# Performance work log

Hardware: AMD Instinct MI355X
Metric: run time of the kernel (lower is better)

The kernel has to match this reference:

```python
import jax, jax.numpy as jnp
import numpy as np
from math import factorial, sqrt

LMAX = 2
NB = 32
NRBF = 20
CUTOFF = 5.0
N_ATOMS = 20000
N_EDGES = 400000
T = 2
M = (LMAX + 1) ** 2
LIDX = np.repeat(np.arange(LMAX + 1), 2 * np.arange(LMAX + 1) + 1)  # l of each flat (l,m) index


def _cg_complex(j1, m1, j2, m2, j3, m3):
    # Racah formula for complex-SH Clebsch-Gordan coefficients
    if m3 != m1 + m2 or j3 < abs(j1 - j2) or j3 > j1 + j2:
        return 0.0
    f = factorial
    pref = sqrt((2 * j3 + 1) * f(j1 + j2 - j3) * f(j1 - j2 + j3) * f(-j1 + j2 + j3) / f(j1 + j2 + j3 + 1))
    pref *= sqrt(f(j1 + m1) * f(j1 - m1) * f(j2 + m2) * f(j2 - m2) * f(j3 + m3) * f(j3 - m3))
    kmin = max(0, j2 - j3 - m1, j1 + m2 - j3)
    kmax = min(j1 + j2 - j3, j1 - m1, j2 + m2)
    s = 0.0
    for k in range(kmin, kmax + 1):
        s += (-1) ** k / (f(k) * f(j1 + j2 - j3 - k) * f(j1 - m1 - k) * f(j2 + m2 - k) * f(j3 - j2 + m1 + k) * f(j3 - j1 - m2 + k))
    return pref * s


def _u_matrix(l):
    # real-SH = U @ complex-SH (rows: real m from -l..l, cols: complex m')
    U = np.zeros((2 * l + 1, 2 * l + 1), dtype=np.complex128)
    for m in range(-l, l + 1):
        if m == 0:
            U[l, l] = 1.0
        elif m > 0:
            U[l + m, l + m] = (-1) ** m / sqrt(2)
            U[l + m, l - m] = 1.0 / sqrt(2)
        else:
            mu = -m
            U[l + m, l + m] = 1j / sqrt(2)
            U[l + m, l - m] = -1j * (-1) ** mu / sqrt(2)
    return U


def _build_cg_rsh(lmax):
    # CG coefficients in the real-SH basis, parity invariant (odd l1+l2+l3 blocks zero)
    cg = np.zeros((M, M, M), dtype=np.float64)
    Us = [_u_matrix(l) for l in range(lmax + 1)]
    for l1 in range(lmax + 1):
        for l2 in range(lmax + 1):
            for l3 in range(lmax + 1):
                if (l1 + l2 + l3) % 2 == 1 or l3 < abs(l1 - l2) or l3 > l1 + l2:
                    continue
                Cc = np.zeros((2 * l1 + 1, 2 * l2 + 1, 2 * l3 + 1), dtype=np.complex128)
                for i, m1 in enumerate(range(-l1, l1 + 1)):
                    for j, m2 in enumerate(range(-l2, l2 + 1)):
                        m3 = m1 + m2
                        if abs(m3) <= l3:
                            Cc[i, j, l3 + m3] = _cg_complex(l1, m1, l2, m2, l3, m3)
                R = np.einsum('ai,bj,ck,ijk->abc', Us[l1], Us[l2], np.conj(Us[l3]), Cc)
                cg[l1 * l1:(l1 + 1) ** 2, l2 * l2:(l2 + 1) ** 2, l3 * l3:(l3 + 1) ** 2] = np.real(R)
    return cg.astype(np.float32)


CG = jnp.asarray(_build_cg_rsh(LMAX))   # [9, 9, 9]
LIDX_J = jnp.asarray(LIDX)


def _rsh(dirs):
    # real spherical harmonics up to l=2 on unit vectors, flat (l,m) order -> [P, 9]
    x, y, z = dirs[:, 0], dirs[:, 1], dirs[:, 2]
    c1 = 0.4886025119029199
    c2 = 1.0925484305920792
    return jnp.stack([
        jnp.full_like(x, 0.28209479177387814),
        c1 * y, c1 * z, c1 * x,
        c2 * x * y, c2 * y * z,
        0.31539156525252005 * (3.0 * z * z - 1.0),
        c2 * x * z,
        0.5462742152960396 * (x * x - y * y),
    ], axis=1)


def _forward(atomic_numbers, r_ij, idx_i, idx_j, emb, Wf, bf, Wm1, Wm2, Wm3, Wg, bg):
    d = jnp.linalg.norm(r_ij, axis=1)                      # [P]
    Y = _rsh(r_ij / d[:, None])                            # [P, 9]
    offsets = jnp.linspace(0.0, CUTOFF, NRBF)
    width = CUTOFF / (NRBF - 1)
    radial = jnp.exp(-0.5 / width ** 2 * (d[:, None] - offsets) ** 2)   # GaussianRBF [P, NRBF]
    fcut = jnp.where(d < CUTOFF, 0.5 * (jnp.cos(d * jnp.pi / CUTOFF) + 1.0), 0.0)  # CosineCutoff
    x0 = emb[atomic_numbers]                               # nuclear embedding [N, NB]
    x = jnp.concatenate([x0[:, None, :], jnp.zeros((x0.shape[0], M - 1, NB), x0.dtype)], axis=1)  # scalar2rsh
    for t in range(T):
        # SO3Convolution: per-edge radial filter per output degree l, cutoff gated
        Wl = ((radial @ Wf[t].T + bf[t]) * fcut[:, None]).reshape(-1, LMAX + 1, NB)
        xj = x[idx_j]                                      # gather neighbors [P, 9, NB]
        tbc = jnp.einsum('pa,abc->pbc', Y, CG)             # contract Y_ij with CG
        yij = jnp.einsum('pbc,pbn->pcn', tbc, xj) * Wl[:, LIDX_J, :]
        dx = jax.ops.segment_sum(yij, idx_i, num_segments=x.shape[0], indices_are_sorted=True)
        ddx = jnp.einsum('xcn,kn->xck', dx, Wm1[t])        # mixing1 (no bias)
        dx = dx + jnp.einsum('abc,xan,xbn->xcn', CG, dx, ddx)  # SO3TensorProduct
        dx = jnp.einsum('xcn,kn->xck', dx, Wm2[t])         # mixing2
        h = jax.nn.sigmoid((dx[:, 0, :] @ Wg[t].T + bg[t]).reshape(-1, LMAX + 1, NB))
        dx = dx * h[:, LIDX_J, :]                          # SO3ParametricGatedNonlinearity
        dx = jnp.einsum('xcn,kn->xck', dx, Wm3[t])         # mixing3
        x = x + dx
    return x                                               # multipole representation [N, 9, NB]


def setup_inputs():
    key = jax.random.key(0)
    ks = jax.random.split(key, 12)
    return {
        'atomic_numbers': jax.random.randint(ks[0], (N_ATOMS,), 1, 100),
        'r_ij': jax.random.normal(ks[1], (N_EDGES, 3), jnp.float32),
        'idx_i': jnp.sort(jax.random.randint(ks[2], (N_EDGES,), 0, N_ATOMS)),
        'idx_j': jax.random.randint(ks[3], (N_EDGES,), 0, N_ATOMS),
        'emb': jax.random.normal(ks[4], (101, NB), jnp.float32).at[0].set(0.0),
        'Wf': jax.random.normal(ks[5], (T, (LMAX + 1) * NB, NRBF), jnp.float32) / sqrt(NRBF),
        'bf': jnp.zeros((T, (LMAX + 1) * NB), jnp.float32),
        'Wm1': jax.random.normal(ks[6], (T, NB, NB), jnp.float32) / sqrt(NB),
        'Wm2': jax.random.normal(ks[7], (T, NB, NB), jnp.float32) / sqrt(NB),
        'Wm3': jax.random.normal(ks[8], (T, NB, NB), jnp.float32) / sqrt(NB),
        'Wg': jax.random.normal(ks[9], (T, (LMAX + 1) * NB, NB), jnp.float32) / sqrt(NB),
        'bg': jnp.zeros((T, (LMAX + 1) * NB), jnp.float32),
    }


def reference(atomic_numbers, r_ij, idx_i, idx_j, emb, Wf, bf, Wm1, Wm2, Wm3, Wg, bg):
    return _forward(atomic_numbers, r_ij, idx_i, idx_j, emb, Wf, bf, Wm1, Wm2, Wm3, Wg, bg)
```

## Files before the change

kernel.cpp:

```cpp
#include <hip/hip_runtime.h>

#define CHUNK 16

constexpr double CFACT[8] = {1.,1.,2.,6.,24.,120.,720.,5040.};

constexpr double csqrt(double x){
  if (x <= 0.0) return 0.0;
  double s = 1.0;
  while (x > 4.0)  { x *= 0.25; s *= 2.0; }
  while (x < 0.25) { x *= 4.0;  s *= 0.5; }
  double g = 1.0;
  for (int i=0;i<10;i++) g = 0.5*(g + x/g);
  return s*g;
}

constexpr double cg_complex(int j1,int m1,int j2,int m2,int j3,int m3){
  if (m3 != m1+m2 || j3 < (j1>j2?j1-j2:j2-j1) || j3 > j1+j2) return 0.0;
  double pref = csqrt((2.0*j3+1.0)*CFACT[j1+j2-j3]*CFACT[j1-j2+j3]*CFACT[-j1+j2+j3]/CFACT[j1+j2+j3+1]);
  pref *= csqrt(CFACT[j1+m1]*CFACT[j1-m1]*CFACT[j2+m2]*CFACT[j2-m2]*CFACT[j3+m3]*CFACT[j3-m3]);
  int kmin = 0;
  if (j2-j3-m1 > kmin) kmin = j2-j3-m1;
  if (j1+m2-j3 > kmin) kmin = j1+m2-j3;
  int kmax = j1+j2-j3;
  if (j1-m1 < kmax) kmax = j1-m1;
  if (j2+m2 < kmax) kmax = j2+m2;
  double s = 0.0;
  for (int k=kmin;k<=kmax;++k){
    double t = 1.0/(CFACT[k]*CFACT[j1+j2-j3-k]*CFACT[j1-m1-k]*CFACT[j2+m2-k]*CFACT[j3-j2+m1+k]*CFACT[j3-j1-m2+k]);
    s += (k&1)? -t : t;
  }
  return pref*s;
}

struct UR { int n; int mc[2]; double re[2]; double im[2]; };
constexpr UR u_row(int m){
  UR u{}; const double is2 = 0.70710678118654752440;
  if (m==0){ u.n=1; u.mc[0]=0; u.re[0]=1.0; u.im[0]=0.0; u.mc[1]=0; u.re[1]=0.0; u.im[1]=0.0; }
  else if (m>0){ u.n=2; u.mc[0]=m;  u.re[0]=((m&1)? -is2:is2); u.im[0]=0.0;
                        u.mc[1]=-m; u.re[1]=is2;               u.im[1]=0.0; }
  else { int mu=-m; u.n=2; u.mc[0]=m;  u.re[0]=0.0; u.im[0]=is2;
                           u.mc[1]=mu; u.re[1]=0.0; u.im[1]=((mu&1)? is2:-is2); }
  return u;
}

struct CGTab { float v[9][9][9]; };
constexpr CGTab build_cg(){
  CGTab g{};
  double cc[9][9][9] = {};
  for (int a=0;a<9;a++){
    int l1 = (a==0)?0:((a<4)?1:2); int m1 = a - (l1*l1+l1);
    for (int b=0;b<9;b++){
      int l2 = (b==0)?0:((b<4)?1:2); int m2 = b - (l2*l2+l2);
      int m3 = m1+m2;
      for (int l3=0;l3<=2;l3++){
        if (m3 < -l3 || m3 > l3) continue;
        cc[a][b][l3*l3+l3+m3] = cg_complex(l1,m1,l2,m2,l3,m3);
      }
    }
  }
  for (int l1=0;l1<=2;l1++) for (int l2=0;l2<=2;l2++) for (int l3=0;l3<=2;l3++){
    if (((l1+l2+l3)&1)==1) continue;
    int dl = (l1>l2)?(l1-l2):(l2-l1);
    if (l3 < dl || l3 > l1+l2) continue;
    for (int m1=-l1;m1<=l1;m1++) for (int m2=-l2;m2<=l2;m2++) for (int m3=-l3;m3<=l3;m3++){
      UR ua = u_row(m1), ub = u_row(m2), uc = u_row(m3);
      double acc = 0.0;
      for (int i=0;i<ua.n;i++) for (int j=0;j<ub.n;j++){
        double zr = ua.re[i]*ub.re[j] - ua.im[i]*ub.im[j];
        double zi = ua.re[i]*ub.im[j] + ua.im[i]*ub.re[j];
        for (int k=0;k<uc.n;k++){
          double rp = zr*uc.re[k] + zi*uc.im[k];
          if (rp != 0.0)
            acc += rp * cc[l1*l1+l1+ua.mc[i]][l2*l2+l2+ub.mc[j]][l3*l3+l3+uc.mc[k]];
        }
      }
      g.v[l1*l1+l1+m1][l2*l2+l2+m2][l3*l3+l3+m3] = (float)acc;
    }
  }
  return g;
}
constexpr CGTab CGT = build_cg();

__global__ void init_x_kernel(const int* __restrict__ Z, const float* __restrict__ emb,
                              float4* __restrict__ x4, float4* __restrict__ dx4, int n_atoms){
  int i = blockIdx.x*blockDim.x + threadIdx.x;
  if (i >= n_atoms*72) return;
  int atom = i/72, rem = i - atom*72;
  float4 v = make_float4(0.f,0.f,0.f,0.f);
  if (rem < 8) v = reinterpret_cast<const float4*>(emb)[Z[atom]*8 + rem];
  x4[i] = v;
  dx4[i] = make_float4(0.f,0.f,0.f,0.f);
}

template<bool FIRST>
__global__ __launch_bounds__(256) void edge_kernel(
    const float* __restrict__ r_ij, const int* __restrict__ idx_i, const int* __restrict__ idx_j,
    const float* __restrict__ x, const float* __restrict__ Wf_t, const float* __restrict__ bf_t,
    float* __restrict__ dx, int n_edges)
{
  int tid = threadIdx.x;
  int g = tid >> 5, lane = tid & 31;

  int base = (blockIdx.x*8 + g)*CHUNK;
  if (base >= n_edges) return;

  int pidx;
  {
    int e0 = base + (lane & 15);
    if (e0 > n_edges-1) e0 = n_edges-1;
    pidx = (lane < 16) ? idx_i[e0] : idx_j[e0];
  }
  float rv0, rv1;
  {
    long long rmax = (long long)n_edges*3 - 1;
    long long a0 = (long long)base*3 + lane;       if (a0 > rmax) a0 = rmax;
    long long a1 = (long long)base*3 + 32 + lane;  if (a1 > rmax) a1 = rmax;
    rv0 = r_ij[a0];
    rv1 = r_ij[a1];
  }

  float wfr[3][20]; float bfl[3];
  #pragma unroll
  for (int l=0;l<3;l++){
    const float* rp = Wf_t + (l*32+lane)*20;
    #pragma unroll
    for (int q=0;q<5;q++){
      float4 v4 = *reinterpret_cast<const float4*>(rp + q*4);
      wfr[l][q*4+0]=v4.x; wfr[l][q*4+1]=v4.y; wfr[l][q*4+2]=v4.z; wfr[l][q*4+3]=v4.w;
    }
    bfl[l] = bf_t[l*32+lane];
  }

  const float STEP  = 5.0f/19.0f;
  const float ALPHA = -0.5f/(STEP*STEP);
  float myoff = (float)lane * STEP;

  float racc[9];
  #pragma unroll
  for (int c=0;c<9;c++) racc[c]=0.f;
  int cur_i = -1;

  float xjn[9];
  float xjn0;
  {
    int j0 = __shfl(pidx, 16, 32);
    const float* xp = x + j0*288 + lane;
    if (FIRST){
      xjn0 = xp[0];
    } else {
      #pragma unroll
      for (int b=0;b<9;b++) xjn[b] = xp[b*32];
    }
  }

  #pragma unroll
  for (int k=0;k<CHUNK;k++){
    int e = base + k;
    if (e >= n_edges) break;

    float xj[9]; float xj0;
    if (FIRST){
      xj0 = xjn0;
    } else {
      #pragma unroll
      for (int b=0;b<9;b++) xj[b] = xjn[b];
    }

    if (k+1 < CHUNK){
      int jn = __shfl(pidx, 16+k+1, 32);
      const float* xp = x + jn*288 + lane;
      if (FIRST){
        xjn0 = xp[0];
      } else {
        #pragma unroll
        for (int b=0;b<9;b++) xjn[b] = xp[b*32];
      }
    }

    int ii = __shfl(pidx, k, 32);

    float rx = (3*k+0 < 32) ? __shfl(rv0, 3*k+0, 32) : __shfl(rv1, 3*k+0-32, 32);
    float ry = (3*k+1 < 32) ? __shfl(rv0, 3*k+1, 32) : __shfl(rv1, 3*k+1-32, 32);
    float rz = (3*k+2 < 32) ? __shfl(rv0, 3*k+2, 32) : __shfl(rv1, 3*k+2-32, 32);

    float d2 = fmaf(rx,rx,fmaf(ry,ry,rz*rz));
    float dd = sqrtf(d2);
    float inv = __fdividef(1.0f, dd);
    float X = rx*inv, Yv = ry*inv, Zv = rz*inv;
    const float c1 = 0.4886025119029199f, c2 = 1.0925484305920792f;
    float Y[9];
    Y[0]=0.28209479177387814f; Y[1]=c1*Yv; Y[2]=c1*Zv; Y[3]=c1*X;
    Y[4]=c2*X*Yv; Y[5]=c2*Yv*Zv; Y[6]=0.31539156525252005f*(3.f*Zv*Zv-1.f);
    Y[7]=c2*X*Zv; Y[8]=0.5462742152960396f*(X*X-Yv*Yv);

    float dtl = dd - myoff;
    float rbl = __expf(ALPHA*dtl*dtl);
    float wl0=bfl[0], wl1=bfl[1], wl2=bfl[2];
    #pragma unroll
    for (int r=0;r<20;r++){
      float rb = __shfl(rbl, r, 32);
      wl0 = fmaf(rb, wfr[0][r], wl0);
      wl1 = fmaf(rb, wfr[1][r], wl1);
      wl2 = fmaf(rb, wfr[2][r], wl2);
    }
    float fc = (dd < 5.0f) ? 0.5f*(__cosf(dd*0.6283185307179586f)+1.0f) : 0.0f;
    wl0*=fc; wl1*=fc; wl2*=fc;

    if (ii != cur_i){
      if (cur_i >= 0){
        float* dp = dx + cur_i*288 + lane;
        #pragma unroll
        for (int c=0;c<9;c++){ atomicAdd(dp + c*32, racc[c]); racc[c]=0.f; }
      }
      cur_i = ii;
    }

    if (FIRST){
      racc[0] = fmaf(wl0, Y[0]*xj0, racc[0]);
      #pragma unroll
      for (int c=1;c<4;c++) racc[c] = fmaf(wl1, Y[c]*xj0, racc[c]);
      #pragma unroll
      for (int c=4;c<9;c++) racc[c] = fmaf(wl2, Y[c]*xj0, racc[c]);
    } else {
      float yv[9];
      #pragma unroll
      for (int c=0;c<9;c++) yv[c]=0.f;
      #pragma unroll
      for (int a=0;a<9;a++){
        #pragma unroll
        for (int b=0;b<9;b++){
          bool any = false;
          #pragma unroll
          for (int c=0;c<9;c++) any = any | (CGT.v[a][b][c] != 0.f);
          if (any){
            float p = Y[a]*xj[b];
            #pragma unroll
            for (int c=0;c<9;c++){
              if (CGT.v[a][b][c] != 0.f) yv[c] = fmaf(CGT.v[a][b][c], p, yv[c]);
            }
          }
        }
      }
      racc[0] = fmaf(wl0, yv[0], racc[0]);
      #pragma unroll
      for (int c=1;c<4;c++) racc[c] = fmaf(wl1, yv[c], racc[c]);
      #pragma unroll
      for (int c=4;c<9;c++) racc[c] = fmaf(wl2, yv[c], racc[c]);
    }
  }
  if (cur_i >= 0){
    float* dp = dx + cur_i*288 + lane;
    #pragma unroll
    for (int c=0;c<9;c++) atomicAdd(dp + c*32, racc[c]);
  }
}

__global__ __launch_bounds__(256) void atom_kernel(
    float* __restrict__ x, float* __restrict__ dxg,
    const float* __restrict__ Wm1_t, const float* __restrict__ Wm2_t, const float* __restrict__ Wm3_t,
    const float* __restrict__ Wg_t, const float* __restrict__ bg_t, int n_atoms)
{
  __shared__ __align__(16) float tile[8][288];
  int tid = threadIdx.x;
  int g = tid>>5, k = tid&31;
  int atom = blockIdx.x*8 + g;
  if (atom >= n_atoms) return;
  float* tg = &tile[g][0];
  const float4* t4 = reinterpret_cast<const float4*>(tg);

  float* dp = dxg + atom*288 + k;
  float v[9];
  #pragma unroll
  for (int c=0;c<9;c++){ v[c]=dp[c*32]; tg[c*32+k]=v[c]; dp[c*32]=0.f; }

  float wr[32];
  {
    const float4* w4 = reinterpret_cast<const float4*>(Wm1_t + k*32);
    #pragma unroll
    for (int q=0;q<8;q++){ float4 a=w4[q]; wr[4*q]=a.x; wr[4*q+1]=a.y; wr[4*q+2]=a.z; wr[4*q+3]=a.w; }
  }
  float u[9];
  #pragma unroll
  for (int c=0;c<9;c++){
    float s=0.f;
    #pragma unroll
    for (int q=0;q<8;q++){
      float4 tv = t4[c*8+q];
      s = fmaf(tv.x, wr[4*q+0], s); s = fmaf(tv.y, wr[4*q+1], s);
      s = fmaf(tv.z, wr[4*q+2], s); s = fmaf(tv.w, wr[4*q+3], s);
    }
    u[c]=s;
  }

  float w[9];
  #pragma unroll
  for (int c=0;c<9;c++) w[c]=v[c];
  #pragma unroll
  for (int a=0;a<9;a++){
    #pragma unroll
    for (int b=0;b<9;b++){
      bool any = false;
      #pragma unroll
      for (int c=0;c<9;c++) any = any | (CGT.v[a][b][c] != 0.f);
      if (any){
        float p = v[a]*u[b];
        #pragma unroll
        for (int c=0;c<9;c++){
          if (CGT.v[a][b][c] != 0.f) w[c] = fmaf(CGT.v[a][b][c], p, w[c]);
        }
      }
    }
  }

  #pragma unroll
  for (int c=0;c<9;c++) tg[c*32+k]=w[c];
  {
    const float4* w4 = reinterpret_cast<const float4*>(Wm2_t + k*32);
    #pragma unroll
    for (int q=0;q<8;q++){ float4 a=w4[q]; wr[4*q]=a.x; wr[4*q+1]=a.y; wr[4*q+2]=a.z; wr[4*q+3]=a.w; }
  }
  float p[9];
  #pragma unroll
  for (int c=0;c<9;c++){
    float s=0.f;
    #pragma unroll
    for (int q=0;q<8;q++){
      float4 tv = t4[c*8+q];
      s = fmaf(tv.x, wr[4*q+0], s); s = fmaf(tv.y, wr[4*q+1], s);
      s = fmaf(tv.z, wr[4*q+2], s); s = fmaf(tv.w, wr[4*q+3], s);
    }
    p[c]=s;
  }

  tg[k] = p[0];
  float s0=bg_t[k], s1=bg_t[32+k], s2=bg_t[64+k];
  {
    const float4* wg0 = reinterpret_cast<const float4*>(Wg_t + (     k)*32);
    const float4* wg1 = reinterpret_cast<const float4*>(Wg_t + (32 + k)*32);
    const float4* wg2 = reinterpret_cast<const float4*>(Wg_t + (64 + k)*32);
    #pragma unroll
    for (int q=0;q<8;q++){
      float4 tv = t4[q];
      float4 a0 = wg0[q], a1 = wg1[q], a2 = wg2[q];
      s0 = fmaf(tv.x,a0.x,s0); s0 = fmaf(tv.y,a0.y,s0); s0 = fmaf(tv.z,a0.z,s0); s0 = fmaf(tv.w,a0.w,s0);
      s1 = fmaf(tv.x,a1.x,s1); s1 = fmaf(tv.y,a1.y,s1); s1 = fmaf(tv.z,a1.z,s1); s1 = fmaf(tv.w,a1.w,s1);
      s2 = fmaf(tv.x,a2.x,s2); s2 = fmaf(tv.y,a2.y,s2); s2 = fmaf(tv.z,a2.z,s2); s2 = fmaf(tv.w,a2.w,s2);
    }
  }
  float h0 = 1.f/(1.f+__expf(-s0));
  float h1 = 1.f/(1.f+__expf(-s1));
  float h2 = 1.f/(1.f+__expf(-s2));

  float q9[9];
  q9[0]=p[0]*h0;
  #pragma unroll
  for (int c=1;c<4;c++) q9[c]=p[c]*h1;
  #pragma unroll
  for (int c=4;c<9;c++) q9[c]=p[c]*h2;

  #pragma unroll
  for (int c=0;c<9;c++) tg[c*32+k]=q9[c];
  {
    const float4* w4 = reinterpret_cast<const float4*>(Wm3_t + k*32);
    #pragma unroll
    for (int q=0;q<8;q++){ float4 a=w4[q]; wr[4*q]=a.x; wr[4*q+1]=a.y; wr[4*q+2]=a.z; wr[4*q+3]=a.w; }
  }
  float* xo = x + atom*288 + k;
  #pragma unroll
  for (int c=0;c<9;c++){
    float s=0.f;
    #pragma unroll
    for (int q=0;q<8;q++){
      float4 tv = t4[c*8+q];
      s = fmaf(tv.x, wr[4*q+0], s); s = fmaf(tv.y, wr[4*q+1], s);
      s = fmaf(tv.z, wr[4*q+2], s); s = fmaf(tv.w, wr[4*q+3], s);
    }
    xo[c*32] += s;
  }
}

extern "C" void kernel_launch(void* const* d_in, const int* in_sizes, int n_in,
                              void* d_out, int out_size, void* d_ws, size_t ws_size,
                              hipStream_t stream)
{
  const int*   Z    = (const int*)d_in[0];
  const float* r_ij = (const float*)d_in[1];
  const int*   idxi = (const int*)d_in[2];
  const int*   idxj = (const int*)d_in[3];
  const float* emb  = (const float*)d_in[4];
  const float* Wf   = (const float*)d_in[5];
  const float* bf   = (const float*)d_in[6];
  const float* Wm1  = (const float*)d_in[7];
  const float* Wm2  = (const float*)d_in[8];
  const float* Wm3  = (const float*)d_in[9];
  const float* Wg   = (const float*)d_in[10];
  const float* bg   = (const float*)d_in[11];
  int n_atoms = in_sizes[0];
  int n_edges = in_sizes[1]/3;

  float* x  = (float*)d_out;
  float* dx = (float*)d_ws;

  init_x_kernel<<<(n_atoms*72+255)/256,256,0,stream>>>(Z, emb, (float4*)x, (float4*)dx, n_atoms);

  int eblocks = (n_edges + 8*CHUNK - 1)/(8*CHUNK);
  int ablocks = (n_atoms + 7)/8;

  edge_kernel<true><<<eblocks,256,0,stream>>>(r_ij, idxi, idxj, x, Wf, bf, dx, n_edges);
  atom_kernel<<<ablocks,256,0,stream>>>(x, dx, Wm1, Wm2, Wm3, Wg, bg, n_atoms);

  edge_kernel<false><<<eblocks,256,0,stream>>>(r_ij, idxi, idxj, x,
                                        Wf + 96*20, bf + 96, dx, n_edges);
  atom_kernel<<<ablocks,256,0,stream>>>(x, dx,
                                        Wm1 + 1024, Wm2 + 1024, Wm3 + 1024,
                                        Wg + 96*32, bg + 96, n_atoms);
}
```

Measured before the change: 414.8 us.

## Drop init kernel, read embeddings directly, stream r_ij per edge, roll edge loop

Removes the init_x kernel. The first edge pass now reads the embedding through Z, and the first atom pass writes x outright, adding the embedding to channel 0 instead of accumulating. dx is zeroed with hipMemsetAsync, and the final atom pass no longer clears dx. The edge loop is no longer unrolled and loads the next edge's r_ij directly instead of shuffling it from a coalesced bulk load, which trades register pressure and code size for more scalar-like global loads.

```diff
diff --git a/kernel.cpp b/kernel.cpp
--- a/kernel.cpp
+++ b/kernel.cpp
@@ -81,21 +81,11 @@
 }
 constexpr CGTab CGT = build_cg();
 
-__global__ void init_x_kernel(const int* __restrict__ Z, const float* __restrict__ emb,
-                              float4* __restrict__ x4, float4* __restrict__ dx4, int n_atoms){
-  int i = blockIdx.x*blockDim.x + threadIdx.x;
-  if (i >= n_atoms*72) return;
-  int atom = i/72, rem = i - atom*72;
-  float4 v = make_float4(0.f,0.f,0.f,0.f);
-  if (rem < 8) v = reinterpret_cast<const float4*>(emb)[Z[atom]*8 + rem];
-  x4[i] = v;
-  dx4[i] = make_float4(0.f,0.f,0.f,0.f);
-}
-
 template<bool FIRST>
 __global__ __launch_bounds__(256) void edge_kernel(
     const float* __restrict__ r_ij, const int* __restrict__ idx_i, const int* __restrict__ idx_j,
-    const float* __restrict__ x, const float* __restrict__ Wf_t, const float* __restrict__ bf_t,
+    const float* __restrict__ x, const int* __restrict__ Z, const float* __restrict__ emb,
+    const float* __restrict__ Wf_t, const float* __restrict__ bf_t,
     float* __restrict__ dx, int n_edges)
 {
   int tid = threadIdx.x;
@@ -110,14 +100,6 @@
     if (e0 > n_edges-1) e0 = n_edges-1;
     pidx = (lane < 16) ? idx_i[e0] : idx_j[e0];
   }
-  float rv0, rv1;
-  {
-    long long rmax = (long long)n_edges*3 - 1;
-    long long a0 = (long long)base*3 + lane;       if (a0 > rmax) a0 = rmax;
-    long long a1 = (long long)base*3 + 32 + lane;  if (a1 > rmax) a1 = rmax;
-    rv0 = r_ij[a0];
-    rv1 = r_ij[a1];
-  }
 
   float wfr[3][20]; float bfl[3];
   #pragma unroll
@@ -140,24 +122,25 @@
   for (int c=0;c<9;c++) racc[c]=0.f;
   int cur_i = -1;
 
-  float xjn[9];
-  float xjn0;
+  float xjn[9]; float xjn0; float rnx, rny, rnz;
   {
     int j0 = __shfl(pidx, 16, 32);
-    const float* xp = x + j0*288 + lane;
     if (FIRST){
-      xjn0 = xp[0];
+      xjn0 = emb[Z[j0]*32 + lane];
     } else {
+      const float* xp = x + j0*288 + lane;
       #pragma unroll
       for (int b=0;b<9;b++) xjn[b] = xp[b*32];
     }
-  }
-
-  #pragma unroll
+    rnx = r_ij[base*3+0]; rny = r_ij[base*3+1]; rnz = r_ij[base*3+2];
+  }
+
+  #pragma unroll 1
   for (int k=0;k<CHUNK;k++){
     int e = base + k;
     if (e >= n_edges) break;
 
+    float rx = rnx, ry = rny, rz = rnz;
     float xj[9]; float xj0;
     if (FIRST){
       xj0 = xjn0;
@@ -165,23 +148,19 @@
       #pragma unroll
       for (int b=0;b<9;b++) xj[b] = xjn[b];
     }
-
-    if (k+1 < CHUNK){
+    int ii = __shfl(pidx, k, 32);
+
+    if (k+1 < CHUNK && e+1 < n_edges){
       int jn = __shfl(pidx, 16+k+1, 32);
-      const float* xp = x + jn*288 + lane;
       if (FIRST){
-        xjn0 = xp[0];
+        xjn0 = emb[Z[jn]*32 + lane];
       } else {
+        const float* xp = x + jn*288 + lane;
         #pragma unroll
         for (int b=0;b<9;b++) xjn[b] = xp[b*32];
       }
-    }
-
-    int ii = __shfl(pidx, k, 32);
-
-    float rx = (3*k+0 < 32) ? __shfl(rv0, 3*k+0, 32) : __shfl(rv1, 3*k+0-32, 32);
-    float ry = (3*k+1 < 32) ? __shfl(rv0, 3*k+1, 32) : __shfl(rv1, 3*k+1-32, 32);
-    float rz = (3*k+2 < 32) ? __shfl(rv0, 3*k+2, 32) : __shfl(rv1, 3*k+2-32, 32);
+      rnx = r_ij[(e+1)*3+0]; rny = r_ij[(e+1)*3+1]; rnz = r_ij[(e+1)*3+2];
+    }
 
     float d2 = fmaf(rx,rx,fmaf(ry,ry,rz*rz));
     float dd = sqrtf(d2);
@@ -255,8 +234,10 @@
   }
 }
 
+template<bool FIRST, bool LAST>
 __global__ __launch_bounds__(256) void atom_kernel(
     float* __restrict__ x, float* __restrict__ dxg,
+    const int* __restrict__ Z, const float* __restrict__ emb,
     const float* __restrict__ Wm1_t, const float* __restrict__ Wm2_t, const float* __restrict__ Wm3_t,
     const float* __restrict__ Wg_t, const float* __restrict__ bg_t, int n_atoms)
 {
@@ -268,10 +249,16 @@
   float* tg = &tile[g][0];
   const float4* t4 = reinterpret_cast<const float4*>(tg);
 
+  float embv;
+  if (FIRST) embv = emb[Z[atom]*32 + k];
+
   float* dp = dxg + atom*288 + k;
   float v[9];
   #pragma unroll
-  for (int c=0;c<9;c++){ v[c]=dp[c*32]; tg[c*32+k]=v[c]; dp[c*32]=0.f; }
+  for (int c=0;c<9;c++){
+    v[c]=dp[c*32]; tg[c*32+k]=v[c];
+    if (!LAST) dp[c*32]=0.f;
+  }
 
   float wr[32];
   {
@@ -375,7 +362,12 @@
       s = fmaf(tv.x, wr[4*q+0], s); s = fmaf(tv.y, wr[4*q+1], s);
       s = fmaf(tv.z, wr[4*q+2], s); s = fmaf(tv.w, wr[4*q+3], s);
     }
-    xo[c*32] += s;
+    if (FIRST){
+      float base = (c==0)? embv : 0.f;
+      xo[c*32] = base + s;
+    } else {
+      xo[c*32] += s;
+    }
   }
 }
 
@@ -401,17 +393,17 @@
   float* x  = (float*)d_out;
   float* dx = (float*)d_ws;
 
-  init_x_kernel<<<(n_atoms*72+255)/256,256,0,stream>>>(Z, emb, (float4*)x, (float4*)dx, n_atoms);
+  hipMemsetAsync(dx, 0, (size_t)n_atoms*288*sizeof(float), stream);
 
   int eblocks = (n_edges + 8*CHUNK - 1)/(8*CHUNK);
   int ablocks = (n_atoms + 7)/8;
 
-  edge_kernel<true><<<eblocks,256,0,stream>>>(r_ij, idxi, idxj, x, Wf, bf, dx, n_edges);
-  atom_kernel<<<ablocks,256,0,stream>>>(x, dx, Wm1, Wm2, Wm3, Wg, bg, n_atoms);
-
-  edge_kernel<false><<<eblocks,256,0,stream>>>(r_ij, idxi, idxj, x,
+  edge_kernel<true><<<eblocks,256,0,stream>>>(r_ij, idxi, idxj, x, Z, emb, Wf, bf, dx, n_edges);
+  atom_kernel<true,false><<<ablocks,256,0,stream>>>(x, dx, Z, emb, Wm1, Wm2, Wm3, Wg, bg, n_atoms);
+
+  edge_kernel<false><<<eblocks,256,0,stream>>>(r_ij, idxi, idxj, x, Z, emb,
                                         Wf + 96*20, bf + 96, dx, n_edges);
-  atom_kernel<<<ablocks,256,0,stream>>>(x, dx,
+  atom_kernel<false,true><<<ablocks,256,0,stream>>>(x, dx, Z, emb,
                                         Wm1 + 1024, Wm2 + 1024, Wm3 + 1024,
                                         Wg + 96*32, bg + 96, n_atoms);
 }
```

Measured after the change: 440.1 us. 1.06x slower.
